# Kernel optimization log

Hardware: AMD Instinct MI355X
Metric: run time of the kernel (lower is better)

Reference implementation:

```python
import jax, jax.numpy as jnp
import numpy as np
import math

D = 256        # embedding_size
NHEAD = 4
HD = D // NHEAD
FF = 2048      # torch TransformerEncoderLayer default dim_feedforward
NLAYER = 3
VOCAB = 30000
OLD = 2048     # resnet50 fc in_features
BPTT = 20
EOS = 2
PAD = 0
MAXLEN = 5000


def make_pe():
    position = np.arange(MAXLEN)[:, None].astype(np.float32)
    div_term = np.exp(np.arange(0, D, 2).astype(np.float32) * (-math.log(10000.0) / D))
    pe = np.zeros((MAXLEN, D), dtype=np.float32)
    pe[:, 0::2] = np.sin(position * div_term)
    pe[:, 1::2] = np.cos(position * div_term)
    return jnp.asarray(pe)  # [maxlen, d]

PE = make_pe()


def setup_inputs() -> dict:
    key = jax.random.key(0)
    ks = jax.random.split(key, 20)
    s = 0.02
    inp = {
        'image_feats': jax.random.normal(ks[0], (64, OLD), jnp.float32),
        'target_ingrs': jax.random.randint(ks[1], (64, BPTT), 0, VOCAB),
        'emb_table': jax.random.normal(ks[2], (VOCAB, D), jnp.float32) * s,
        'W_g2e': jax.random.normal(ks[3], (OLD, D), jnp.float32) * s,
        'b_g2e': jnp.zeros((D,), jnp.float32),
        'W_out': jax.random.normal(ks[4], (D, VOCAB), jnp.float32) * s,
        'b_out': jnp.zeros((VOCAB,), jnp.float32),
    }
    # per-layer transformer params
    Wqkv, bqkv, Wo, bo, W1, b1, W2, b2, g1, be1, g2, be2 = ([] for _ in range(12))
    k = ks[5]
    for l in range(NLAYER):
        k, *sub = jax.random.split(k, 7)
        Wqkv.append(jax.random.normal(sub[0], (D, 3 * D), jnp.float32) * s)
        bqkv.append(jnp.zeros((3 * D,), jnp.float32))
        Wo.append(jax.random.normal(sub[1], (D, D), jnp.float32) * s)
        bo.append(jnp.zeros((D,), jnp.float32))
        W1.append(jax.random.normal(sub[2], (D, FF), jnp.float32) * s)
        b1.append(jnp.zeros((FF,), jnp.float32))
        W2.append(jax.random.normal(sub[3], (FF, D), jnp.float32) * s)
        b2.append(jnp.zeros((D,), jnp.float32))
        g1.append(jnp.ones((D,), jnp.float32)); be1.append(jnp.zeros((D,), jnp.float32))
        g2.append(jnp.ones((D,), jnp.float32)); be2.append(jnp.zeros((D,), jnp.float32))
    stk = lambda xs: jnp.stack(xs)
    inp.update(Wqkv=stk(Wqkv), bqkv=stk(bqkv), Wo=stk(Wo), bo=stk(bo),
               W1=stk(W1), b1=stk(b1), W2=stk(W2), b2=stk(b2),
               g1=stk(g1), be1=stk(be1), g2=stk(g2), be2=stk(be2))
    return inp


def layernorm(x, g, b):
    mu = jnp.mean(x, -1, keepdims=True)
    var = jnp.var(x, -1, keepdims=True)
    return (x - mu) * jax.lax.rsqrt(var + 1e-5) * g + b


def encoder(x, params):
    # x: [S, B, D] (seq-first like torch). Post-norm encoder, ReLU FFN, no mask.
    (Wqkv, bqkv, Wo, bo, W1, b1, W2, b2, g1, be1, g2, be2) = params
    S, B, _ = x.shape
    for l in range(NLAYER):
        qkv = x @ Wqkv[l] + bqkv[l]                  # [S,B,3D]
        q, k, v = jnp.split(qkv, 3, axis=-1)
        def heads(t):  # [S,B,D] -> [B,H,S,hd]
            return t.reshape(S, B, NHEAD, HD).transpose(1, 2, 0, 3)
        q, k, v = heads(q), heads(k), heads(v)
        att = jnp.einsum('bhqd,bhkd->bhqk', q, k) / math.sqrt(HD)
        att = jax.nn.softmax(att, axis=-1)
        o = jnp.einsum('bhqk,bhkd->bhqd', att, v)    # [B,H,S,hd]
        o = o.transpose(2, 0, 1, 3).reshape(S, B, D)
        x = layernorm(x + o @ Wo[l] + bo[l], g1[l], be1[l])
        ff = jax.nn.relu(x @ W1[l] + b1[l]) @ W2[l] + b2[l]
        x = layernorm(x + ff, g2[l], be2[l])
    return x


def mask_from_eos_after(ids):
    # mult_before=False: mask[:,idx] = all(ids[:,1:idx+1] != EOS); mask[:,0]=1
    ne = (ids != EOS)
    ne = ne.at[:, 0].set(True)
    return jnp.cumprod(ne.astype(jnp.int32), axis=1)  # [B,S]


def reference(image_feats, target_ingrs, emb_table, W_g2e, b_g2e, W_out, b_out,
              Wqkv, bqkv, Wo, bo, W1, b1, W2, b2, g1, be1, g2, be2):
    params = (Wqkv, bqkv, Wo, bo, W1, b1, W2, b2, g1, be1, g2, be2)
    B = image_feats.shape[0]
    img_embed = image_feats @ W_g2e + b_g2e          # [B,D]
    bptt = target_ingrs.shape[1]

    # embeds buffer: [bptt, B, D]; position 0 = image embed (note: original code
    # never applies pos_encoder in predict(), so neither do we)
    embeds = jnp.zeros((bptt, B, D), jnp.float32).at[0].set(img_embed)

    probs_steps = []
    words_steps = []
    # loop over decode steps (fixed-length Python loop; each step re-encodes prefix,
    # faithful to original no-KV-cache behavior)
    for i in range(bptt):
        seq = embeds[: i + 1]                        # [i+1, B, D]
        out = encoder(seq, params)[-1]               # [B, D]
        logits = out @ W_out + b_out                 # [B, V]
        sm = jax.nn.softmax(logits, axis=-1)
        widx = jnp.argmax(sm, axis=-1)               # [B]
        probs_steps.append(sm)
        words_steps.append(widx)
        if i + 1 < bptt:
            embeds = embeds.at[i + 1].set(emb_table[widx])

    decoder_out = jnp.stack(probs_steps, axis=1)     # [B, bptt, V]
    sampled_word = jnp.stack(words_steps, axis=1)    # [B, bptt]
    eos = decoder_out[:, :, EOS]
    mask = mask_from_eos_after(target_ingrs)         # [B, bptt] int
    ingr_probs = jnp.max(decoder_out * mask[:, :, None].astype(jnp.float32), axis=1)
    sampled_word = jnp.where(mask == 0, PAD, sampled_word)
    return ingr_probs, sampled_word, eos
```

## Files before the change

### kernel.cpp

```cpp
#include <hip/hip_runtime.h>
#include <math.h>

#define D 256
#define NH 4
#define HDIM 64
#define FFD 2048
#define NL 3
#define VOC 30000
#define BPTT 20
#define BATCH 64
#define NMAX (BPTT*BATCH)

__global__ void k_mask(const int* __restrict__ ids, int* __restrict__ mask) {
  int b = threadIdx.x;
  int run = 1;
  for (int j = 0; j < BPTT; ++j) {
    if (j > 0 && ids[b*BPTT + j] == 2) run = 0;
    mask[b*BPTT + j] = run;
  }
}

__global__ __launch_bounds__(256) void k_img(const float* __restrict__ feats,
                                             const float* __restrict__ Wg,
                                             const float* __restrict__ bg,
                                             float* __restrict__ embeds) {
  __shared__ float xs[2048];
  int b = blockIdx.x, tid = threadIdx.x;
  for (int j = 0; j < 8; ++j) xs[tid + j*256] = feats[b*2048 + tid + j*256];
  __syncthreads();
  float acc = 0.f;
  for (int k = 0; k < 2048; k += 4) {
    float4 xv = *(const float4*)&xs[k];
    acc += xv.x * Wg[(k+0)*D + tid];
    acc += xv.y * Wg[(k+1)*D + tid];
    acc += xv.z * Wg[(k+2)*D + tid];
    acc += xv.w * Wg[(k+3)*D + tid];
  }
  embeds[b*D + tid] = acc + bg[tid];
}

__global__ __launch_bounds__(256) void k_gemm8(
    const float* __restrict__ A, int lda,
    const float* __restrict__ W,
    const float* __restrict__ bias,
    float* __restrict__ C, long pstride,
    int klen, int M, int relu)
{
  __shared__ float As[8][256];
  const int tid  = threadIdx.x;
  const int tok0 = blockIdx.x * 8;
  const int colb = blockIdx.y * 256;
  const int z    = blockIdx.z;
  const int kbeg = z * klen;
  C += (long)z * pstride;
  const int colg = tid & 63;
  const int tokg = tid >> 6;
  const int col  = colb + colg*4;
  int colL = col;
  if (colL > M-4) colL = M-4;

  float acc[2][4] = {{0.f,0.f,0.f,0.f},{0.f,0.f,0.f,0.f}};

  for (int k0 = 0; k0 < klen; k0 += 256) {
    __syncthreads();
#pragma unroll
    for (int j = 0; j < 8; ++j)
      As[j][tid] = A[(long)(tok0 + j)*lda + kbeg + k0 + tid];
    __syncthreads();
    const float* Wp = W + (long)(kbeg + k0)*M + colL;
#pragma unroll 2
    for (int kk = 0; kk < 256; kk += 4) {
      float a[2][4], w[4][4];
      *(float4*)a[0] = *(const float4*)&As[tokg*2+0][kk];
      *(float4*)a[1] = *(const float4*)&As[tokg*2+1][kk];
      *(float4*)w[0] = *(const float4*)(Wp + (long)(kk+0)*M);
      *(float4*)w[1] = *(const float4*)(Wp + (long)(kk+1)*M);
      *(float4*)w[2] = *(const float4*)(Wp + (long)(kk+2)*M);
      *(float4*)w[3] = *(const float4*)(Wp + (long)(kk+3)*M);
#pragma unroll
      for (int j = 0; j < 2; ++j)
#pragma unroll
        for (int c = 0; c < 4; ++c)
#pragma unroll
          for (int q = 0; q < 4; ++q)
            acc[j][c] += a[j][q] * w[q][c];
    }
  }

  if (col < M) {
    float bv[4] = {0.f,0.f,0.f,0.f};
    if (bias) *(float4*)bv = *(const float4*)(bias + col);
#pragma unroll
    for (int j = 0; j < 2; ++j) {
      float v[4];
#pragma unroll
      for (int c = 0; c < 4; ++c) {
        v[c] = acc[j][c] + bv[c];
        if (relu) v[c] = fmaxf(v[c], 0.f);
      }
      *(float4*)(C + (long)(tok0 + tokg*2 + j)*M + col) = *(float4*)v;
    }
  }
}

__global__ __launch_bounds__(256) void k_resln(
    const float* __restrict__ x, const float* __restrict__ parts, int nparts, long pstride,
    const float* __restrict__ bias, const float* __restrict__ g, const float* __restrict__ be,
    float* __restrict__ out)
{
  __shared__ float red[4];
  int tok = blockIdx.x, tid = threadIdx.x;
  float v = x[(long)tok*D + tid] + bias[tid];
  for (int p = 0; p < nparts; ++p) v += parts[(long)p*pstride + (long)tok*D + tid];

  float s = v;
  for (int off = 32; off; off >>= 1) s += __shfl_down(s, off);
  if ((tid & 63) == 0) red[tid >> 6] = s;
  __syncthreads();
  float mu = (red[0]+red[1]+red[2]+red[3]) * (1.0f/D);
  __syncthreads();
  float dv = v - mu;
  float q = dv*dv;
  for (int off = 32; off; off >>= 1) q += __shfl_down(q, off);
  if ((tid & 63) == 0) red[tid >> 6] = q;
  __syncthreads();
  float var = (red[0]+red[1]+red[2]+red[3]) * (1.0f/D);
  float inv = 1.0f / sqrtf(var + 1e-5f);
  out[(long)tok*D + tid] = dv * inv * g[tid] + be[tid];
}

__global__ __launch_bounds__(64) void k_attn(const float* __restrict__ qkv,
                                             float* __restrict__ o, int S)
{
  __shared__ float qs[BPTT*HDIM], ks[BPTT*HDIM], vs[BPTT*HDIM], ps[BPTT*(BPTT+1)];
  int bh = blockIdx.x;
  int b = bh & 63, h = bh >> 6;
  int d = threadIdx.x;
  for (int s = 0; s < S; ++s) {
    long base = (long)(s*BATCH + b)*(3*D) + h*HDIM + d;
    qs[s*HDIM+d] = qkv[base];
    ks[s*HDIM+d] = qkv[base + D];
    vs[s*HDIM+d] = qkv[base + 2*D];
  }
  __syncthreads();
  for (int p = d; p < S*S; p += 64) {
    int si = p / S, ti = p - si*S;
    float acc = 0.f;
#pragma unroll 4
    for (int k = 0; k < HDIM; ++k) acc += qs[si*HDIM+k] * ks[ti*HDIM+k];
    ps[si*(BPTT+1)+ti] = acc * 0.125f;
  }
  __syncthreads();
  if (d < S) {
    float m = -1e30f;
    for (int t = 0; t < S; ++t) m = fmaxf(m, ps[d*(BPTT+1)+t]);
    float sum = 0.f;
    for (int t = 0; t < S; ++t) { float e = expf(ps[d*(BPTT+1)+t] - m); ps[d*(BPTT+1)+t] = e; sum += e; }
    float inv = 1.0f / sum;
    for (int t = 0; t < S; ++t) ps[d*(BPTT+1)+t] *= inv;
  }
  __syncthreads();
  for (int s = 0; s < S; ++s) {
    float acc = 0.f;
    for (int t = 0; t < S; ++t) acc += ps[s*(BPTT+1)+t] * vs[t*HDIM+d];
    o[(long)(s*BATCH+b)*D + h*HDIM + d] = acc;
  }
}

__global__ __launch_bounds__(256) void k_vocab(
    const float* __restrict__ logits, const int* __restrict__ mask,
    float* __restrict__ out_probs, float* __restrict__ out_words, float* __restrict__ out_eos,
    const float* __restrict__ emb, float* __restrict__ embeds, int step)
{
  __shared__ float redA[4];
  __shared__ float r_s[4];
  __shared__ float r_em[4];
  __shared__ int   r_ei[4];
  int b = blockIdx.x, tid = threadIdx.x;
  const float* lrow = logits + (long)b*VOC;

  float m = -1e30f;
  for (int c = tid; c < VOC; c += 256) m = fmaxf(m, lrow[c]);
  for (int off = 32; off; off >>= 1) m = fmaxf(m, __shfl_down(m, off));
  if ((tid & 63) == 0) redA[tid >> 6] = m;
  __syncthreads();
  float gmax = fmaxf(fmaxf(redA[0],redA[1]), fmaxf(redA[2],redA[3]));
  __syncthreads();

  float s = 0.f, em = -1.0f;
  int ei = VOC;
  for (int c = tid; c < VOC; c += 256) {
    float e = expf(lrow[c] - gmax);
    s += e;
    if (e > em) { em = e; ei = c; }
  }
  for (int off = 32; off; off >>= 1) {
    float em2 = __shfl_down(em, off);
    int   ei2 = __shfl_down(ei, off);
    if (em2 > em || (em2 == em && ei2 < ei)) { em = em2; ei = ei2; }
    s += __shfl_down(s, off);
  }
  if ((tid & 63) == 0) { r_s[tid>>6] = s; r_em[tid>>6] = em; r_ei[tid>>6] = ei; }
  __syncthreads();
  float Ssum = r_s[0]+r_s[1]+r_s[2]+r_s[3];
  em = r_em[0]; ei = r_ei[0];
  for (int w = 1; w < 4; ++w)
    if (r_em[w] > em || (r_em[w] == em && r_ei[w] < ei)) { em = r_em[w]; ei = r_ei[w]; }

  int mk = mask[b*BPTT + step];

  for (int c = tid; c < VOC; c += 256) {
    float p = expf(lrow[c] - gmax) / Ssum;
    float* op = out_probs + (long)b*VOC + c;
    if (step == 0) *op = p;
    else if (mk)   *op = fmaxf(*op, p);
    if (c == 2) out_eos[b*BPTT + step] = p;
  }
  if (tid == 0) out_words[b*BPTT + step] = mk ? (float)ei : 0.0f;
  if (step + 1 < BPTT)
    embeds[(long)((step+1)*BATCH + b)*D + tid] = emb[(long)ei*D + tid];
}

extern "C" void kernel_launch(void* const* d_in, const int* in_sizes, int n_in,
                              void* d_out, int out_size, void* d_ws, size_t ws_size,
                              hipStream_t stream) {
  const float* image_feats = (const float*)d_in[0];
  const int*   target      = (const int*)  d_in[1];
  const float* emb_table   = (const float*)d_in[2];
  const float* W_g2e       = (const float*)d_in[3];
  const float* b_g2e       = (const float*)d_in[4];
  const float* W_out       = (const float*)d_in[5];
  const float* b_out       = (const float*)d_in[6];
  const float* Wqkv        = (const float*)d_in[7];
  const float* bqkv        = (const float*)d_in[8];
  const float* Wo          = (const float*)d_in[9];
  const float* bo          = (const float*)d_in[10];
  const float* W1          = (const float*)d_in[11];
  const float* b1          = (const float*)d_in[12];
  const float* W2          = (const float*)d_in[13];
  const float* b2          = (const float*)d_in[14];
  const float* g1          = (const float*)d_in[15];
  const float* be1         = (const float*)d_in[16];
  const float* g2          = (const float*)d_in[17];
  const float* be2         = (const float*)d_in[18];

  float* out_probs = (float*)d_out;
  float* out_words = out_probs + (long)BATCH*VOC;
  float* out_eos   = out_words + BATCH*BPTT;

  char* ws = (char*)d_ws;
  float* embeds = (float*)ws;  ws += sizeof(float)*(long)NMAX*D;
  float* xbuf   = (float*)ws;  ws += sizeof(float)*(long)NMAX*D;
  float* qkvb   = (float*)ws;  ws += sizeof(float)*(long)NMAX*3*D;
  float* obuf   = (float*)ws;  ws += sizeof(float)*(long)NMAX*D;
  float* pbuf   = (float*)ws;  ws += sizeof(float)*(long)4*NMAX*D;
  float* ffb    = (float*)ws;  ws += sizeof(float)*(long)NMAX*FFD;
  float* logits = (float*)ws;  ws += sizeof(float)*(long)BATCH*VOC;
  int*   maskb  = (int*)ws;    ws += sizeof(int)*BATCH*BPTT;

  k_mask<<<1, 64, 0, stream>>>(target, maskb);
  k_img<<<64, 256, 0, stream>>>(image_feats, W_g2e, b_g2e, embeds);

  for (int i = 0; i < BPTT; ++i) {
    int N = (i+1)*BATCH;
    for (int l = 0; l < NL; ++l) {
      const float* X = (l == 0) ? embeds : xbuf;
      k_gemm8<<<dim3(N/8, 3, 1), 256, 0, stream>>>(X, D, Wqkv + (long)l*D*3*D, bqkv + (long)l*3*D,
                                                   qkvb, 0, D, 3*D, 0);
      k_attn<<<dim3(BATCH*NH), 64, 0, stream>>>(qkvb, obuf, i+1);
      k_gemm8<<<dim3(N/8, 1, 1), 256, 0, stream>>>(obuf, D, Wo + (long)l*D*D, nullptr,
                                                   pbuf, 0, D, D, 0);
      k_resln<<<dim3(N), 256, 0, stream>>>(X, pbuf, 1, 0, bo + (long)l*D, g1 + (long)l*D, be1 + (long)l*D, xbuf);
      k_gemm8<<<dim3(N/8, FFD/256, 1), 256, 0, stream>>>(xbuf, D, W1 + (long)l*D*FFD, b1 + (long)l*FFD,
                                                         ffb, 0, D, FFD, 1);
      k_gemm8<<<dim3(N/8, 1, 4), 256, 0, stream>>>(ffb, FFD, W2 + (long)l*FFD*D, nullptr,
                                                   pbuf, (long)NMAX*D, FFD/4, D, 0);
      k_resln<<<dim3(N), 256, 0, stream>>>(xbuf, pbuf, 4, (long)NMAX*D, b2 + (long)l*D, g2 + (long)l*D, be2 + (long)l*D, xbuf);
    }
    k_gemm8<<<dim3(BATCH/8, (VOC+255)/256, 1), 256, 0, stream>>>(xbuf + (long)i*BATCH*D, D, W_out, b_out,
                                                                 logits, 0, D, VOC, 0);
    k_vocab<<<dim3(BATCH), 256, 0, stream>>>(logits, maskb, out_probs, out_words, out_eos,
                                             emb_table, embeds, i);
  }
}
```

Measured before the change: 10.89 ms.

## Fuse QKV projection into attention and layernorm into projection GEMMs

```diff
diff --git a/kernel.cpp b/kernel.cpp
--- a/kernel.cpp
+++ b/kernel.cpp
@@ -11,21 +11,21 @@
 #define BATCH 64
 #define NMAX (BPTT*BATCH)
 
-__global__ void k_mask(const int* __restrict__ ids, int* __restrict__ mask) {
-  int b = threadIdx.x;
-  int run = 1;
-  for (int j = 0; j < BPTT; ++j) {
-    if (j > 0 && ids[b*BPTT + j] == 2) run = 0;
-    mask[b*BPTT + j] = run;
-  }
-}
-
 __global__ __launch_bounds__(256) void k_img(const float* __restrict__ feats,
                                              const float* __restrict__ Wg,
                                              const float* __restrict__ bg,
-                                             float* __restrict__ embeds) {
+                                             float* __restrict__ embeds,
+                                             const int* __restrict__ ids,
+                                             int* __restrict__ mask) {
   __shared__ float xs[2048];
   int b = blockIdx.x, tid = threadIdx.x;
+  if (b == 0 && tid < 64) {
+    int run = 1;
+    for (int j = 0; j < BPTT; ++j) {
+      if (j > 0 && ids[tid*BPTT + j] == 2) run = 0;
+      mask[tid*BPTT + j] = run;
+    }
+  }
   for (int j = 0; j < 8; ++j) xs[tid + j*256] = feats[b*2048 + tid + j*256];
   __syncthreads();
   float acc = 0.f;
@@ -39,52 +39,45 @@
   embeds[b*D + tid] = acc + bg[tid];
 }
 
-__global__ __launch_bounds__(256) void k_gemm8(
+__global__ __launch_bounds__(256) void k_gemm(
     const float* __restrict__ A, int lda,
     const float* __restrict__ W,
     const float* __restrict__ bias,
-    float* __restrict__ C, long pstride,
-    int klen, int M, int relu)
-{
-  __shared__ float As[8][256];
+    float* __restrict__ C, int M, int relu)
+{
+  __shared__ float As[2048];
   const int tid  = threadIdx.x;
   const int tok0 = blockIdx.x * 8;
   const int colb = blockIdx.y * 256;
-  const int z    = blockIdx.z;
-  const int kbeg = z * klen;
-  C += (long)z * pstride;
   const int colg = tid & 63;
   const int tokg = tid >> 6;
   const int col  = colb + colg*4;
-  int colL = col;
-  if (colL > M-4) colL = M-4;
+  int colL = col; if (colL > M-4) colL = M-4;
 
   float acc[2][4] = {{0.f,0.f,0.f,0.f},{0.f,0.f,0.f,0.f}};
 
-  for (int k0 = 0; k0 < klen; k0 += 256) {
-    __syncthreads();
-#pragma unroll
-    for (int j = 0; j < 8; ++j)
-      As[j][tid] = A[(long)(tok0 + j)*lda + kbeg + k0 + tid];
-    __syncthreads();
-    const float* Wp = W + (long)(kbeg + k0)*M + colL;
+  __syncthreads();
+#pragma unroll
+  for (int j = 0; j < 8; ++j)
+    As[j*256 + tid] = A[(long)(tok0 + j)*lda + tid];
+  __syncthreads();
+  const float* Wp = W + colL;
 #pragma unroll 2
-    for (int kk = 0; kk < 256; kk += 4) {
-      float a[2][4], w[4][4];
-      *(float4*)a[0] = *(const float4*)&As[tokg*2+0][kk];
-      *(float4*)a[1] = *(const float4*)&As[tokg*2+1][kk];
-      *(float4*)w[0] = *(const float4*)(Wp + (long)(kk+0)*M);
-      *(float4*)w[1] = *(const float4*)(Wp + (long)(kk+1)*M);
-      *(float4*)w[2] = *(const float4*)(Wp + (long)(kk+2)*M);
-      *(float4*)w[3] = *(const float4*)(Wp + (long)(kk+3)*M);
-#pragma unroll
-      for (int j = 0; j < 2; ++j)
-#pragma unroll
-        for (int c = 0; c < 4; ++c)
-#pragma unroll
-          for (int q = 0; q < 4; ++q)
-            acc[j][c] += a[j][q] * w[q][c];
-    }
+  for (int kk = 0; kk < 256; kk += 4) {
+    float a0[4], a1[4], w[4][4];
+    *(float4*)a0   = *(const float4*)&As[(tokg*2+0)*256 + kk];
+    *(float4*)a1   = *(const float4*)&As[(tokg*2+1)*256 + kk];
+    *(float4*)w[0] = *(const float4*)(Wp + (long)(kk+0)*M);
+    *(float4*)w[1] = *(const float4*)(Wp + (long)(kk+1)*M);
+    *(float4*)w[2] = *(const float4*)(Wp + (long)(kk+2)*M);
+    *(float4*)w[3] = *(const float4*)(Wp + (long)(kk+3)*M);
+#pragma unroll
+    for (int c = 0; c < 4; ++c)
+#pragma unroll
+      for (int q = 0; q < 4; ++q) {
+        acc[0][c] += a0[q] * w[q][c];
+        acc[1][c] += a1[q] * w[q][c];
+      }
   }
 
   if (col < M) {
@@ -103,68 +96,191 @@
   }
 }
 
-__global__ __launch_bounds__(256) void k_resln(
-    const float* __restrict__ x, const float* __restrict__ parts, int nparts, long pstride,
-    const float* __restrict__ bias, const float* __restrict__ g, const float* __restrict__ be,
+__global__ __launch_bounds__(256) void k_attn2(const float* __restrict__ X,
+                                               const float* __restrict__ Wqkv_l,
+                                               const float* __restrict__ bqkv_l,
+                                               float* __restrict__ o, int S)
+{
+  __shared__ float xs[BPTT*256];
+  __shared__ float qs[BPTT*68], ks[BPTT*68], vs[BPTT*68];
+  __shared__ float ps[BPTT*21];
+  const int unit = blockIdx.x, b = unit & 63, h = unit >> 6, tid = threadIdx.x;
+
+  for (int idx = tid; idx < S*256; idx += 256) {
+    int s = idx >> 8, k = idx & 255;
+    xs[idx] = X[(long)(s*BATCH + b)*D + k];
+  }
+  __syncthreads();
+
+  if (tid < 192) {
+    const int j = tid >> 6, dd = tid & 63;
+    const int colW = j*D + h*HDIM + dd;
+    float acc[BPTT];
+#pragma unroll
+    for (int s = 0; s < BPTT; ++s) acc[s] = 0.f;
+    for (int k = 0; k < 256; ++k) {
+      float w = Wqkv_l[(long)k*(3*D) + colW];
+#pragma unroll
+      for (int s = 0; s < BPTT; ++s) acc[s] += xs[s*256 + k] * w;
+    }
+    float bqv = bqkv_l[colW];
+    float* dst = (j == 0) ? qs : (j == 1) ? ks : vs;
+#pragma unroll
+    for (int s = 0; s < BPTT; ++s) dst[s*68 + dd] = acc[s] + bqv;
+  }
+  __syncthreads();
+
+  for (int p = tid; p < S*S; p += 256) {
+    int si = p / S, ti = p - si*S;
+    float a = 0.f;
+#pragma unroll 8
+    for (int k = 0; k < HDIM; ++k) a += qs[si*68 + k] * ks[ti*68 + k];
+    ps[si*21 + ti] = a * 0.125f;
+  }
+  __syncthreads();
+  if (tid < S) {
+    float m = -1e30f;
+    for (int t = 0; t < S; ++t) m = fmaxf(m, ps[tid*21 + t]);
+    float sum = 0.f;
+    for (int t = 0; t < S; ++t) { float e = expf(ps[tid*21 + t] - m); ps[tid*21 + t] = e; sum += e; }
+    float inv = 1.0f / sum;
+    for (int t = 0; t < S; ++t) ps[tid*21 + t] *= inv;
+  }
+  __syncthreads();
+  for (int idx = tid; idx < S*HDIM; idx += 256) {
+    int s = idx >> 6, dd = idx & 63;
+    float a = 0.f;
+    for (int t = 0; t < S; ++t) a += ps[s*21 + t] * vs[t*68 + dd];
+    o[(long)(s*BATCH + b)*D + h*HDIM + dd] = a;
+  }
+}
+
+__global__ __launch_bounds__(256) void k_projln(
+    const float* __restrict__ Aop, const float* __restrict__ W,
+    const float* __restrict__ X, const float* __restrict__ bias,
+    const float* __restrict__ g, const float* __restrict__ be,
     float* __restrict__ out)
 {
-  __shared__ float red[4];
-  int tok = blockIdx.x, tid = threadIdx.x;
-  float v = x[(long)tok*D + tid] + bias[tid];
-  for (int p = 0; p < nparts; ++p) v += parts[(long)p*pstride + (long)tok*D + tid];
-
-  float s = v;
-  for (int off = 32; off; off >>= 1) s += __shfl_down(s, off);
-  if ((tid & 63) == 0) red[tid >> 6] = s;
-  __syncthreads();
-  float mu = (red[0]+red[1]+red[2]+red[3]) * (1.0f/D);
-  __syncthreads();
-  float dv = v - mu;
-  float q = dv*dv;
-  for (int off = 32; off; off >>= 1) q += __shfl_down(q, off);
-  if ((tid & 63) == 0) red[tid >> 6] = q;
-  __syncthreads();
-  float var = (red[0]+red[1]+red[2]+red[3]) * (1.0f/D);
-  float inv = 1.0f / sqrtf(var + 1e-5f);
-  out[(long)tok*D + tid] = dv * inv * g[tid] + be[tid];
-}
-
-__global__ __launch_bounds__(64) void k_attn(const float* __restrict__ qkv,
-                                             float* __restrict__ o, int S)
-{
-  __shared__ float qs[BPTT*HDIM], ks[BPTT*HDIM], vs[BPTT*HDIM], ps[BPTT*(BPTT+1)];
-  int bh = blockIdx.x;
-  int b = bh & 63, h = bh >> 6;
-  int d = threadIdx.x;
-  for (int s = 0; s < S; ++s) {
-    long base = (long)(s*BATCH + b)*(3*D) + h*HDIM + d;
-    qs[s*HDIM+d] = qkv[base];
-    ks[s*HDIM+d] = qkv[base + D];
-    vs[s*HDIM+d] = qkv[base + 2*D];
-  }
-  __syncthreads();
-  for (int p = d; p < S*S; p += 64) {
-    int si = p / S, ti = p - si*S;
-    float acc = 0.f;
+  __shared__ float As[2048];
+  const int tid  = threadIdx.x;
+  const int tok0 = blockIdx.x * 8;
+  const int colg = tid & 63;
+  const int tokg = tid >> 6;
+  const int col  = colg*4;
+
+  float acc[2][4] = {{0.f,0.f,0.f,0.f},{0.f,0.f,0.f,0.f}};
+
+  __syncthreads();
+#pragma unroll
+  for (int j = 0; j < 8; ++j)
+    As[j*256 + tid] = Aop[(long)(tok0 + j)*D + tid];
+  __syncthreads();
+  const float* Wp = W + col;
+#pragma unroll 2
+  for (int kk = 0; kk < 256; kk += 4) {
+    float a0[4], a1[4], w[4][4];
+    *(float4*)a0   = *(const float4*)&As[(tokg*2+0)*256 + kk];
+    *(float4*)a1   = *(const float4*)&As[(tokg*2+1)*256 + kk];
+    *(float4*)w[0] = *(const float4*)(Wp + (long)(kk+0)*D);
+    *(float4*)w[1] = *(const float4*)(Wp + (long)(kk+1)*D);
+    *(float4*)w[2] = *(const float4*)(Wp + (long)(kk+2)*D);
+    *(float4*)w[3] = *(const float4*)(Wp + (long)(kk+3)*D);
+#pragma unroll
+    for (int c = 0; c < 4; ++c)
+#pragma unroll
+      for (int q = 0; q < 4; ++q) {
+        acc[0][c] += a0[q] * w[q][c];
+        acc[1][c] += a1[q] * w[q][c];
+      }
+  }
+
+  float bv[4], gv[4], bev[4];
+  *(float4*)bv  = *(const float4*)(bias + col);
+  *(float4*)gv  = *(const float4*)(g + col);
+  *(float4*)bev = *(const float4*)(be + col);
+
+#pragma unroll
+  for (int j = 0; j < 2; ++j) {
+    const int tok = tok0 + tokg*2 + j;
+    float v[4];
+    float4 xv = *(const float4*)(X + (long)tok*D + col);
+    v[0] = acc[j][0] + bv[0] + xv.x;
+    v[1] = acc[j][1] + bv[1] + xv.y;
+    v[2] = acc[j][2] + bv[2] + xv.z;
+    v[3] = acc[j][3] + bv[3] + xv.w;
+    float s = v[0]+v[1]+v[2]+v[3];
+#pragma unroll
+    for (int off = 1; off < 64; off <<= 1) s += __shfl_xor(s, off);
+    float mu = s * (1.0f/D);
+    float q0=v[0]-mu, q1=v[1]-mu, q2=v[2]-mu, q3=v[3]-mu;
+    float q = q0*q0+q1*q1+q2*q2+q3*q3;
+#pragma unroll
+    for (int off = 1; off < 64; off <<= 1) q += __shfl_xor(q, off);
+    float inv = 1.0f / sqrtf(q * (1.0f/D) + 1e-5f);
+    float ov[4];
+    ov[0] = q0*inv*gv[0] + bev[0];
+    ov[1] = q1*inv*gv[1] + bev[1];
+    ov[2] = q2*inv*gv[2] + bev[2];
+    ov[3] = q3*inv*gv[3] + bev[3];
+    *(float4*)(out + (long)tok*D + col) = *(float4*)ov;
+  }
+}
+
+__global__ __launch_bounds__(256) void k_ff2ln(
+    const float* __restrict__ ff, const float* __restrict__ W2,
+    const float* __restrict__ x1, const float* __restrict__ b2,
+    const float* __restrict__ g, const float* __restrict__ be,
+    float* __restrict__ out)
+{
+  __shared__ float As[4*260];
+  const int tid  = threadIdx.x;
+  const int tok0 = blockIdx.x * 4;
+  const int wave = tid >> 6;
+  const int lane = tid & 63;
+  const int col  = lane * 4;
+
+  float acc[4] = {0.f,0.f,0.f,0.f};
+
+  for (int k0 = 0; k0 < FFD; k0 += 256) {
+    __syncthreads();
+    {
+      int r = tid >> 6, c = (tid & 63) * 4;
+      *(float4*)&As[r*260 + c] = *(const float4*)&ff[(long)(tok0 + r)*FFD + k0 + c];
+    }
+    __syncthreads();
+    const float* Wp = W2 + (long)k0*D + col;
 #pragma unroll 4
-    for (int k = 0; k < HDIM; ++k) acc += qs[si*HDIM+k] * ks[ti*HDIM+k];
-    ps[si*(BPTT+1)+ti] = acc * 0.125f;
-  }
-  __syncthreads();
-  if (d < S) {
-    float m = -1e30f;
-    for (int t = 0; t < S; ++t) m = fmaxf(m, ps[d*(BPTT+1)+t]);
-    float sum = 0.f;
-    for (int t = 0; t < S; ++t) { float e = expf(ps[d*(BPTT+1)+t] - m); ps[d*(BPTT+1)+t] = e; sum += e; }
-    float inv = 1.0f / sum;
-    for (int t = 0; t < S; ++t) ps[d*(BPTT+1)+t] *= inv;
-  }
-  __syncthreads();
-  for (int s = 0; s < S; ++s) {
-    float acc = 0.f;
-    for (int t = 0; t < S; ++t) acc += ps[s*(BPTT+1)+t] * vs[t*HDIM+d];
-    o[(long)(s*BATCH+b)*D + h*HDIM + d] = acc;
-  }
+    for (int kk = 0; kk < 256; ++kk) {
+      float a = As[wave*260 + kk];
+      float4 w = *(const float4*)(Wp + (long)kk*D);
+      acc[0] += a*w.x; acc[1] += a*w.y; acc[2] += a*w.z; acc[3] += a*w.w;
+    }
+  }
+
+  const int tok = tok0 + wave;
+  float bv[4], gv[4], bev[4], xv[4];
+  *(float4*)bv  = *(const float4*)(b2 + col);
+  *(float4*)gv  = *(const float4*)(g + col);
+  *(float4*)bev = *(const float4*)(be + col);
+  *(float4*)xv  = *(const float4*)(x1 + (long)tok*D + col);
+  float v[4];
+#pragma unroll
+  for (int c = 0; c < 4; ++c) v[c] = acc[c] + bv[c] + xv[c];
+  float s = v[0]+v[1]+v[2]+v[3];
+#pragma unroll
+  for (int off = 1; off < 64; off <<= 1) s += __shfl_xor(s, off);
+  float mu = s * (1.0f/D);
+  float q0=v[0]-mu, q1=v[1]-mu, q2=v[2]-mu, q3=v[3]-mu;
+  float q = q0*q0+q1*q1+q2*q2+q3*q3;
+#pragma unroll
+  for (int off = 1; off < 64; off <<= 1) q += __shfl_xor(q, off);
+  float inv = 1.0f / sqrtf(q * (1.0f/D) + 1e-5f);
+  float ov[4];
+  ov[0] = q0*inv*gv[0] + bev[0];
+  ov[1] = q1*inv*gv[1] + bev[1];
+  ov[2] = q2*inv*gv[2] + bev[2];
+  ov[3] = q3*inv*gv[3] + bev[3];
+  *(float4*)(out + (long)tok*D + col) = *(float4*)ov;
 }
 
 __global__ __launch_bounds__(256) void k_vocab(
@@ -172,19 +288,17 @@
     float* __restrict__ out_probs, float* __restrict__ out_words, float* __restrict__ out_eos,
     const float* __restrict__ emb, float* __restrict__ embeds, int step)
 {
-  __shared__ float redA[4];
-  __shared__ float r_s[4];
-  __shared__ float r_em[4];
-  __shared__ int   r_ei[4];
+  __shared__ float redf[12];
+  __shared__ int   redi[4];
   int b = blockIdx.x, tid = threadIdx.x;
   const float* lrow = logits + (long)b*VOC;
 
   float m = -1e30f;
   for (int c = tid; c < VOC; c += 256) m = fmaxf(m, lrow[c]);
   for (int off = 32; off; off >>= 1) m = fmaxf(m, __shfl_down(m, off));
-  if ((tid & 63) == 0) redA[tid >> 6] = m;
-  __syncthreads();
-  float gmax = fmaxf(fmaxf(redA[0],redA[1]), fmaxf(redA[2],redA[3]));
+  if ((tid & 63) == 0) redf[tid >> 6] = m;
+  __syncthreads();
+  float gmax = fmaxf(fmaxf(redf[0],redf[1]), fmaxf(redf[2],redf[3]));
   __syncthreads();
 
   float s = 0.f, em = -1.0f;
@@ -200,15 +314,14 @@
     if (em2 > em || (em2 == em && ei2 < ei)) { em = em2; ei = ei2; }
     s += __shfl_down(s, off);
   }
-  if ((tid & 63) == 0) { r_s[tid>>6] = s; r_em[tid>>6] = em; r_ei[tid>>6] = ei; }
-  __syncthreads();
-  float Ssum = r_s[0]+r_s[1]+r_s[2]+r_s[3];
-  em = r_em[0]; ei = r_ei[0];
+  if ((tid & 63) == 0) { redf[4+(tid>>6)] = s; redf[8+(tid>>6)] = em; redi[tid>>6] = ei; }
+  __syncthreads();
+  float Ssum = redf[4]+redf[5]+redf[6]+redf[7];
+  em = redf[8]; ei = redi[0];
   for (int w = 1; w < 4; ++w)
-    if (r_em[w] > em || (r_em[w] == em && r_ei[w] < ei)) { em = r_em[w]; ei = r_ei[w]; }
+    if (redf[8+w] > em || (redf[8+w] == em && redi[w] < ei)) { em = redf[8+w]; ei = redi[w]; }
 
   int mk = mask[b*BPTT + step];
-
   for (int c = tid; c < VOC; c += 256) {
     float p = expf(lrow[c] - gmax) / Ssum;
     float* op = out_probs + (long)b*VOC + c;
@@ -251,34 +364,28 @@
   char* ws = (char*)d_ws;
   float* embeds = (float*)ws;  ws += sizeof(float)*(long)NMAX*D;
   float* xbuf   = (float*)ws;  ws += sizeof(float)*(long)NMAX*D;
-  float* qkvb   = (float*)ws;  ws += sizeof(float)*(long)NMAX*3*D;
   float* obuf   = (float*)ws;  ws += sizeof(float)*(long)NMAX*D;
-  float* pbuf   = (float*)ws;  ws += sizeof(float)*(long)4*NMAX*D;
   float* ffb    = (float*)ws;  ws += sizeof(float)*(long)NMAX*FFD;
   float* logits = (float*)ws;  ws += sizeof(float)*(long)BATCH*VOC;
   int*   maskb  = (int*)ws;    ws += sizeof(int)*BATCH*BPTT;
 
-  k_mask<<<1, 64, 0, stream>>>(target, maskb);
-  k_img<<<64, 256, 0, stream>>>(image_feats, W_g2e, b_g2e, embeds);
+  k_img<<<BATCH, 256, 0, stream>>>(image_feats, W_g2e, b_g2e, embeds, target, maskb);
 
   for (int i = 0; i < BPTT; ++i) {
-    int N = (i+1)*BATCH;
+    const int S = i + 1, N = S * BATCH, ntt = N / 8;
     for (int l = 0; l < NL; ++l) {
       const float* X = (l == 0) ? embeds : xbuf;
-      k_gemm8<<<dim3(N/8, 3, 1), 256, 0, stream>>>(X, D, Wqkv + (long)l*D*3*D, bqkv + (long)l*3*D,
-                                                   qkvb, 0, D, 3*D, 0);
-      k_attn<<<dim3(BATCH*NH), 64, 0, stream>>>(qkvb, obuf, i+1);
-      k_gemm8<<<dim3(N/8, 1, 1), 256, 0, stream>>>(obuf, D, Wo + (long)l*D*D, nullptr,
-                                                   pbuf, 0, D, D, 0);
-      k_resln<<<dim3(N), 256, 0, stream>>>(X, pbuf, 1, 0, bo + (long)l*D, g1 + (long)l*D, be1 + (long)l*D, xbuf);
-      k_gemm8<<<dim3(N/8, FFD/256, 1), 256, 0, stream>>>(xbuf, D, W1 + (long)l*D*FFD, b1 + (long)l*FFD,
-                                                         ffb, 0, D, FFD, 1);
-      k_gemm8<<<dim3(N/8, 1, 4), 256, 0, stream>>>(ffb, FFD, W2 + (long)l*FFD*D, nullptr,
-                                                   pbuf, (long)NMAX*D, FFD/4, D, 0);
-      k_resln<<<dim3(N), 256, 0, stream>>>(xbuf, pbuf, 4, (long)NMAX*D, b2 + (long)l*D, g2 + (long)l*D, be2 + (long)l*D, xbuf);
-    }
-    k_gemm8<<<dim3(BATCH/8, (VOC+255)/256, 1), 256, 0, stream>>>(xbuf + (long)i*BATCH*D, D, W_out, b_out,
-                                                                 logits, 0, D, VOC, 0);
+      k_attn2<<<dim3(BATCH*NH), 256, 0, stream>>>(X, Wqkv + (long)l*D*3*D, bqkv + (long)l*3*D,
+                                                  obuf, S);
+      k_projln<<<dim3(ntt), 256, 0, stream>>>(obuf, Wo + (long)l*D*D, X, bo + (long)l*D,
+                                              g1 + (long)l*D, be1 + (long)l*D, xbuf);
+      k_gemm<<<dim3(ntt, FFD/256), 256, 0, stream>>>(xbuf, D, W1 + (long)l*D*FFD, b1 + (long)l*FFD,
+                                                     ffb, FFD, 1);
+      k_ff2ln<<<dim3(N/4), 256, 0, stream>>>(ffb, W2 + (long)l*FFD*D, xbuf, b2 + (long)l*D,
+                                             g2 + (long)l*D, be2 + (long)l*D, xbuf);
+    }
+    k_gemm<<<dim3(8, (VOC+255)/256), 256, 0, stream>>>(xbuf + (long)i*BATCH*D, D, W_out, b_out,
+                                                       logits, VOC, 0);
     k_vocab<<<dim3(BATCH), 256, 0, stream>>>(logits, maskb, out_probs, out_words, out_eos,
                                              emb_table, embeds, i);
   }
```

Result: slower. 17.24 ms (+58.3%).
